# Kernel tuning notes

Measured on AMD Instinct MI355X. Metric: run time of the kernel, lower is better.

## Reference

```python
import math
import jax, jax.numpy as jnp
import numpy as np

B, S, E = 4, 2048, 768
H, D = 12, 64
LOCAL_H, GLOBAL_H = 8, 4
WINDOW_BASE, MIN_W, MAX_W = 128, 32, 512
GLOBAL_RATIO = 0.1
MASK_VALUE = -1e9


def setup_inputs() -> dict:
    key = jax.random.key(0)
    k1, k2, k3 = jax.random.split(key, 3)
    return {
        "x": jax.random.normal(k1, (B, S, E), dtype=jnp.float32),
        "w_attn": jax.random.normal(k2, (E, 3 * E), dtype=jnp.float32) * 0.02,
        "b_attn": jnp.zeros((3 * E,), dtype=jnp.float32),
        "w_proj": jax.random.normal(k3, (E, E), dtype=jnp.float32) * 0.02,
        "b_proj": jnp.zeros((E,), dtype=jnp.float32),
    }


def _masks(seq_len: int):
    # dynamic window (adaptive): base * sqrt(S/base), clamped
    w = int(WINDOW_BASE * math.sqrt(seq_len / WINDOW_BASE))
    w = max(MIN_W, min(w, MAX_W))
    half = w // 2
    i = jnp.arange(seq_len)[:, None]
    j = jnp.arange(seq_len)[None, :]
    # local: window band then causal override -> allowed iff i-half <= j <= i
    local_allowed = (j >= i - half) & (j <= i)
    local_mask = jnp.where(local_allowed, 0.0, MASK_VALUE).astype(jnp.float32)
    # global: columns at linspace positions allowed for all rows, plus full causal
    n_glob = max(1, int(seq_len * GLOBAL_RATIO))
    gpos = jnp.linspace(0.0, seq_len - 1, n_glob).astype(jnp.int32)
    is_gcol = jnp.zeros((seq_len,), dtype=bool).at[gpos].set(True)
    global_allowed = (j <= i) | is_gcol[None, :]
    global_mask = jnp.where(global_allowed, 0.0, MASK_VALUE).astype(jnp.float32)
    return local_mask, global_mask


def _attend(q, k, v, mask):
    # q,k,v: [B,h,S,D]; mask: [S,S]
    scale = 1.0 / math.sqrt(q.shape[-1])
    scores = jnp.einsum("bhqd,bhkd->bhqk", q, k) * scale + mask[None, None]
    w = jax.nn.softmax(scores, axis=-1)
    return jnp.einsum("bhqk,bhkd->bhqd", w, v)


def reference(x, w_attn, b_attn, w_proj, b_proj):
    b, s, _ = x.shape
    qkv = x @ w_attn + b_attn                       # [B,S,3E]
    q, k, v = jnp.split(qkv, 3, axis=-1)
    def heads(t):
        return t.reshape(b, s, H, D).transpose(0, 2, 1, 3)  # [B,H,S,D]
    q, k, v = heads(q), heads(k), heads(v)
    local_mask, global_mask = _masks(s)
    local_out = _attend(q[:, :LOCAL_H], k[:, :LOCAL_H], v[:, :LOCAL_H], local_mask)
    global_out = _attend(q[:, LOCAL_H:], k[:, LOCAL_H:], v[:, LOCAL_H:], global_mask)
    attn = jnp.concatenate([local_out, global_out], axis=1)  # heads 0..7 local, 8..11 global
    attn = attn.transpose(0, 2, 1, 3).reshape(b, s, E)
    return attn @ w_proj + b_proj
```

## Files before the change

### kernel.cpp

```cpp
#include <hip/hip_runtime.h>
#include <stdint.h>


#define NH 12
#define SQ 2048

typedef __bf16 bf16x8 __attribute__((ext_vector_type(8)));
typedef float f32x4 __attribute__((ext_vector_type(4)));

#define GLOAD_LDS16(g, l)                                                      \
  __builtin_amdgcn_global_load_lds(                                            \
      (__attribute__((address_space(1))) void*)(g),                            \
      (__attribute__((address_space(3))) void*)(l), 16, 0, 0)

__device__ __forceinline__ unsigned short bfbits(float f) {
  __bf16 h = (__bf16)f;
  return *(unsigned short*)&h;
}

__global__ __launch_bounds__(256) void prep(
    const float* __restrict__ x, unsigned short* __restrict__ xb,
    const float* __restrict__ w_attn, unsigned short* __restrict__ wattnT,
    const float* __restrict__ w_proj, unsigned short* __restrict__ wprojT) {
  const int bid = blockIdx.x, t = threadIdx.x;
  if (bid < 512) {
    const int n4 = 8192 * 768 / 4;
    for (int i = bid * 256 + t; i < n4; i += 512 * 256) {
      float4 v = ((const float4*)x)[i];
      ((ushort4*)xb)[i] = make_ushort4(bfbits(v.x), bfbits(v.y), bfbits(v.z), bfbits(v.w));
    }
    return;
  }
  __shared__ float tile[32][33];
  const float* in; unsigned short* out; int K, N, tl;
  if (bid < 512 + 72 * 24) { in = w_attn; out = wattnT; K = 768; N = 2304; tl = bid - 512; }
  else                     { in = w_proj; out = wprojT; K = 768; N = 768;  tl = bid - 512 - 72 * 24; }
  const int tpr = N / 32;
  const int n0 = (tl % tpr) * 32, k0 = (tl / tpr) * 32;
  const int tx = t & 31, ty = t >> 5;
  for (int r = ty; r < 32; r += 8) tile[r][tx] = in[(size_t)(k0 + r) * N + n0 + tx];
  __syncthreads();
  for (int r = ty; r < 32; r += 8) out[(size_t)(n0 + r) * K + k0 + tx] = bfbits(tile[tx][r]);
}

__global__ __launch_bounds__(256) void vprep(const unsigned short* __restrict__ QKV,
                                             unsigned short* __restrict__ Vtb,
                                             unsigned short* __restrict__ Kg,
                                             unsigned short* __restrict__ VgT,
                                             int* __restrict__ gidx) {
  const int id = blockIdx.x, t = threadIdx.x;
  if (id < 1536) {
    const int bh = id >> 5, b = bh / NH, h = bh % NH;
    const int s0 = (id & 31) * 64;
    __shared__ unsigned short T[64][72];
    const int r = t >> 2, c0 = (t & 3) * 16;
    const size_t src = (size_t)(b * SQ + s0 + r) * 2304 + 1536 + h * 64 + c0;
    *(uint4*)&T[r][c0]     = *(const uint4*)&QKV[src];
    *(uint4*)&T[r][c0 + 8] = *(const uint4*)&QKV[src + 8];
    __syncthreads();
    unsigned short pk[16];
#pragma unroll
    for (int z = 0; z < 16; ++z) pk[z] = T[c0 + z][r];
    size_t dst = (size_t)bh * 131072 + (size_t)r * 2048 + s0 + c0;
    *(uint4*)&Vtb[dst]     = *(uint4*)&pk[0];
    *(uint4*)&Vtb[dst + 8] = *(uint4*)&pk[8];
    return;
  }
  const int g = id - 1536;
  const int bh = g >> 3, y = g & 7;
  const int b = bh >> 2, h = 8 + (bh & 3);
  if (g == 0) {
    int c = t;
    gidx[c] = (c < 203) ? (int)((double)c * (2047.0 / 203.0)) : ((c == 203) ? 2047 : -1);
  }
  {
    int c = t, ch = y;
    int col = (c < 203) ? (int)((double)c * (2047.0 / 203.0)) : ((c == 203) ? 2047 : -1);
    uint4 v = {0u, 0u, 0u, 0u};
    if (col >= 0) v = *(const uint4*)&QKV[(size_t)(b * SQ + col) * 2304 + 768 + h * 64 + ch * 8];
    *(uint4*)&Kg[((size_t)bh * 256 + c) * 64 + ch * 8] = v;
  }
  {
    int d = t >> 2;
    int cb = (t & 3) * 64 + y * 8;
    for (int cc = 0; cc < 8; ++cc) {
      int c = cb + cc;
      int col = (c < 203) ? (int)((double)c * (2047.0 / 203.0)) : ((c == 203) ? 2047 : -1);
      unsigned short v = 0;
      if (col >= 0) v = QKV[(size_t)(b * SQ + col) * 2304 + 1536 + h * 64 + d];
      VgT[((size_t)bh * 64 + d) * 256 + c] = v;
    }
  }
}

__device__ __forceinline__ void gemm_mainloop(
    const unsigned short* __restrict__ A, const unsigned short* __restrict__ BT,
    int m0, int n0, int tid,
    unsigned short* As, unsigned short* Bs,
    f32x4 acc[4][4]) {
  const int lane = tid & 63, wave = tid >> 6;
  const int wm = wave >> 1, wn = wave & 1;
  const int ln = lane & 15, quad = lane >> 4;
  const int arow = wave * 16 + (lane >> 2);
  const int acol = (lane & 3) * 8;

#pragma unroll
  for (int mi = 0; mi < 4; ++mi)
#pragma unroll
    for (int ni = 0; ni < 4; ++ni) acc[mi][ni] = (f32x4){0.f, 0.f, 0.f, 0.f};

  for (int kt = 0; kt < 12; ++kt) {
    const int k0 = kt * 64;
    __syncthreads();
#pragma unroll
    for (int p = 0; p < 2; ++p) {
      const int ldso = (p * 64 + wave * 16) * 32;
      GLOAD_LDS16(A  + (size_t)(m0 + p * 64 + arow) * 768 + k0 + acol,       &As[ldso]);
      GLOAD_LDS16(A  + (size_t)(m0 + p * 64 + arow) * 768 + k0 + 32 + acol,  &As[4096 + ldso]);
      GLOAD_LDS16(BT + (size_t)(n0 + p * 64 + arow) * 768 + k0 + acol,       &Bs[ldso]);
      GLOAD_LDS16(BT + (size_t)(n0 + p * 64 + arow) * 768 + k0 + 32 + acol,  &Bs[4096 + ldso]);
    }
    __syncthreads();
#pragma unroll
    for (int kh = 0; kh < 2; ++kh) {
      const int base = kh * 4096;
      bf16x8 aF[4], bF[4];
#pragma unroll
      for (int mi = 0; mi < 4; ++mi)
        aF[mi] = *(const bf16x8*)&As[base + (wm * 64 + mi * 16 + ln) * 32 + quad * 8];
#pragma unroll
      for (int ni = 0; ni < 4; ++ni)
        bF[ni] = *(const bf16x8*)&Bs[base + (wn * 64 + ni * 16 + ln) * 32 + quad * 8];
#pragma unroll
      for (int mi = 0; mi < 4; ++mi)
#pragma unroll
        for (int ni = 0; ni < 4; ++ni)
          acc[mi][ni] = __builtin_amdgcn_mfma_f32_16x16x32_bf16(aF[mi], bF[ni], acc[mi][ni], 0, 0, 0);
    }
  }
}

__global__ __launch_bounds__(256) void qkv_gemm(
    const unsigned short* __restrict__ Xb, const unsigned short* __restrict__ WT,
    const float* __restrict__ bias, unsigned short* __restrict__ Out) {
  __shared__ __attribute__((aligned(16))) unsigned short As[2 * 128 * 32];
  __shared__ __attribute__((aligned(16))) unsigned short Bs[2 * 128 * 32];
  f32x4 acc[4][4];
  const int wg = (blockIdx.x & 7) * 144 + (blockIdx.x >> 3);
  const int m0 = (wg / 18) * 128, n0 = (wg % 18) * 128;
  const int tid = threadIdx.x;
  gemm_mainloop(Xb, WT, m0, n0, tid, As, Bs, acc);
  const int lane = tid & 63, wave = tid >> 6;
  const int wm = wave >> 1, wn = wave & 1, ln = lane & 15, quad = lane >> 4;
#pragma unroll
  for (int mi = 0; mi < 4; ++mi)
#pragma unroll
    for (int ni = 0; ni < 4; ++ni) {
      int n = n0 + wn * 64 + ni * 16 + ln;
      float bs = bias[n];
#pragma unroll
      for (int rg = 0; rg < 4; ++rg) {
        int m = m0 + wm * 64 + mi * 16 + quad * 4 + rg;
        Out[(size_t)m * 2304 + n] = bfbits(acc[mi][ni][rg] + bs);
      }
    }
}

__global__ __launch_bounds__(256) void proj_gemm(
    const unsigned short* __restrict__ Ab, const unsigned short* __restrict__ WT,
    const float* __restrict__ bias, float* __restrict__ Out) {
  __shared__ __attribute__((aligned(16))) unsigned short As[2 * 128 * 32];
  __shared__ __attribute__((aligned(16))) unsigned short Bs[2 * 128 * 32];
  f32x4 acc[4][4];
  const int wg = (blockIdx.x & 7) * 48 + (blockIdx.x >> 3);
  const int m0 = (wg / 6) * 128, n0 = (wg % 6) * 128;
  const int tid = threadIdx.x;
  gemm_mainloop(Ab, WT, m0, n0, tid, As, Bs, acc);
  const int lane = tid & 63, wave = tid >> 6;
  const int wm = wave >> 1, wn = wave & 1, ln = lane & 15, quad = lane >> 4;
#pragma unroll
  for (int mi = 0; mi < 4; ++mi)
#pragma unroll
    for (int ni = 0; ni < 4; ++ni)
#pragma unroll
      for (int rg = 0; rg < 4; ++rg) {
        int m = m0 + wm * 64 + mi * 16 + quad * 4 + rg;
        int n = n0 + wn * 64 + ni * 16 + ln;
        Out[(size_t)m * 768 + n] = acc[mi][ni][rg] + bias[n];
      }
}

__global__ __launch_bounds__(256, 4) void attn_kernel(
    const unsigned short* __restrict__ QKV,
    const unsigned short* __restrict__ Vtb,
    const unsigned short* __restrict__ Kg, const unsigned short* __restrict__ VgT,
    const int* __restrict__ gidx,
    unsigned short* __restrict__ AOut,
    unsigned short* __restrict__ Opart,
    float* __restrict__ Lpart) {
  __shared__ __attribute__((aligned(16))) unsigned short Ks[64 * 64];
  __shared__ __attribute__((aligned(16))) unsigned short Vs[64 * 64];
  __shared__ __attribute__((aligned(16))) unsigned short Ps[64 * 64];

  const int gid = blockIdx.x;
  int b, h, qb, vt0, vt1;
  bool multi = false;
  if (gid < 1536) {
    int bh = gid / 96, rem = gid % 96;
    b = bh >> 2; h = 8 + (bh & 3);
    int part;
    if (rem < 4)       { qb = rem;                               part = 0; }
    else if (rem < 20) { int z = rem - 4;  qb = 4 + (z >> 1);    part = z & 1; }
    else if (rem < 44) { int z = rem - 20; int q = z / 3; qb = 12 + q; part = z - 3 * q; }
    else if (rem < 76) { int z = rem - 44; qb = 20 + (z >> 2);   part = z & 3; }
    else               { int z = rem - 76; int q = z / 5; qb = 28 + q; part = z - 5 * q; }
    vt0 = part * 8;
    vt1 = min(vt0 + 8, qb + 5);
    multi = (qb >= 4);
  } else {
    int lid = gid - 1536;
    int bh = lid >> 5; b = bh >> 3; h = bh & 7; qb = lid & 31;
    vt0 = ((qb > 4) ? qb - 4 : 0) + 4;
    vt1 = qb + 5;
  }
  const int qb0 = qb * 64;
  const bool is_local = (h < 8);
  const int tid = threadIdx.x, lane = tid & 63, wave = tid >> 6;
  const int ln = lane & 15, quad = lane >> 4;
  const int bh48 = b * NH + h;
  const int bhg = (b << 2) | (h & 3);

  const size_t qoff = (size_t)(b * SQ + qb0 + wave * 16 + ln) * 2304 + h * 64;
  bf16x8 qA0 = *(const bf16x8*)&QKV[qoff + quad * 8];
  bf16x8 qA1 = *(const bf16x8*)&QKV[qoff + 32 + quad * 8];

  bf16x8 onesF;
#pragma unroll
  for (int z = 0; z < 8; ++z) onesF[z] = (__bf16)1.0f;

  f32x4 o[4];
  f32x4 ls = (f32x4){0.f, 0.f, 0.f, 0.f};
#pragma unroll
  for (int dt = 0; dt < 4; ++dt) o[dt] = (f32x4){0.f, 0.f, 0.f, 0.f};

  const int irow = qb0 + wave * 16 + quad * 4;
  const int iw = qb0 + wave * 16;
  const int sr = tid >> 3, sch = tid & 7;
  const int ssw = (sch ^ (sr & 7)) * 8;
  const int s0k = (quad ^ (ln & 7)) * 8;
  const int s1k = ((quad + 4) ^ (ln & 7)) * 8;
  const int lnh = ln >> 3, ln7 = ln & 7;

  const float S2 = 0.125f * 1.44269504f, B2 = 8.0f * 1.44269504f;

  uint4 pk0, pk1, pv0, pv1;
  auto issue_load = [&](int vt) {
    if (vt >= 4) {
      const int kstart = (vt - 4) * 64;
      const size_t ko = (size_t)(b * SQ + kstart + sr) * 2304 + 768 + h * 64 + sch * 8;
      pk0 = *(const uint4*)&QKV[ko];
      pk1 = *(const uint4*)&QKV[ko + (size_t)32 * 2304];
      const size_t vo = (size_t)bh48 * 131072 + (size_t)sr * 2048 + kstart + sch * 8;
      pv0 = *(const uint4*)&Vtb[vo];
      pv1 = *(const uint4*)&Vtb[vo + 32 * 2048];
    } else {
      const int kg0 = vt * 64;
      pk0 = *(const uint4*)&Kg[((size_t)bhg * 256 + kg0 + sr) * 64 + sch * 8];
      pk1 = *(const uint4*)&Kg[((size_t)bhg * 256 + kg0 + 32 + sr) * 64 + sch * 8];
      pv0 = *(const uint4*)&VgT[((size_t)bhg * 64 + sr) * 256 + kg0 + sch * 8];
      pv1 = *(const uint4*)&VgT[((size_t)bhg * 64 + 32 + sr) * 256 + kg0 + sch * 8];
    }
  };
  issue_load(vt0);

  for (int vt = vt0; vt < vt1; ++vt) {
    const bool gph = (vt < 4);
    __syncthreads();
    *(uint4*)&Ks[sr * 64 + ssw]        = pk0;
    *(uint4*)&Ks[(32 + sr) * 64 + ssw] = pk1;
    *(uint4*)&Vs[sr * 64 + ssw]        = pv0;
    *(uint4*)&Vs[(32 + sr) * 64 + ssw] = pv1;
    __syncthreads();
    if (vt + 1 < vt1) issue_load(vt + 1);

    const int kstart = (vt - 4) * 64;
    const int kg0 = vt * 64;
    float sc[4][4];
    const bool full = !gph && (kstart + 63 <= iw) && (!is_local || kstart >= iw - 241);
#pragma unroll
    for (int nt = 0; nt < 4; ++nt) {
      bf16x8 kF0 = *(const bf16x8*)&Ks[(nt * 16 + ln) * 64 + s0k];
      bf16x8 kF1 = *(const bf16x8*)&Ks[(nt * 16 + ln) * 64 + s1k];
      f32x4 c = (f32x4){0.f, 0.f, 0.f, 0.f};
      c = __builtin_amdgcn_mfma_f32_16x16x32_bf16(qA0, kF0, c, 0, 0, 0);
      c = __builtin_amdgcn_mfma_f32_16x16x32_bf16(qA1, kF1, c, 0, 0, 0);
      if (full) {
#pragma unroll
        for (int rg = 0; rg < 4; ++rg) sc[nt][rg] = c[rg] * S2 - B2;
      } else if (!gph) {
        int j = kstart + nt * 16 + ln;
#pragma unroll
        for (int rg = 0; rg < 4; ++rg) {
          int i = irow + rg;
          bool ok = is_local ? (j >= i - 256 && j <= i) : (j <= i);
          sc[nt][rg] = ok ? (c[rg] * S2 - B2) : -1e9f;
        }
      } else {
        int jg = gidx[kg0 + nt * 16 + ln];
#pragma unroll
        for (int rg = 0; rg < 4; ++rg) {
          bool ok = jg > (irow + rg);
          sc[nt][rg] = ok ? (c[rg] * S2 - B2) : -1e9f;
        }
      }
    }

    __bf16* P = (__bf16*)Ps;
#pragma unroll
    for (int rg = 0; rg < 4; ++rg) {
      int prow = wave * 16 + quad * 4 + rg;
      int pbase = prow * 64 + ln7;
      int pr7 = prow & 7;
#pragma unroll
      for (int nt = 0; nt < 4; ++nt)
        P[pbase + (((nt * 2 + lnh) ^ pr7) << 3)] = (__bf16)exp2f(sc[nt][rg]);
    }
    bf16x8 pF0 = *(const bf16x8*)&Ps[(wave * 16 + ln) * 64 + s0k];
    bf16x8 pF1 = *(const bf16x8*)&Ps[(wave * 16 + ln) * 64 + s1k];
    ls = __builtin_amdgcn_mfma_f32_16x16x32_bf16(pF0, onesF, ls, 0, 0, 0);
    ls = __builtin_amdgcn_mfma_f32_16x16x32_bf16(pF1, onesF, ls, 0, 0, 0);
#pragma unroll
    for (int dt = 0; dt < 4; ++dt) {
      bf16x8 vF0 = *(const bf16x8*)&Vs[(dt * 16 + ln) * 64 + s0k];
      bf16x8 vF1 = *(const bf16x8*)&Vs[(dt * 16 + ln) * 64 + s1k];
      o[dt] = __builtin_amdgcn_mfma_f32_16x16x32_bf16(pF0, vF0, o[dt], 0, 0, 0);
      o[dt] = __builtin_amdgcn_mfma_f32_16x16x32_bf16(pF1, vF1, o[dt], 0, 0, 0);
    }
  }

  if (gid >= 1536 || !multi) {
#pragma unroll
    for (int dt = 0; dt < 4; ++dt)
#pragma unroll
      for (int rg = 0; rg < 4; ++rg) {
        int row = b * SQ + qb0 + wave * 16 + quad * 4 + rg;
        int e = h * 64 + dt * 16 + ln;
        AOut[(size_t)row * 768 + e] = bfbits(o[dt][rg] / ls[rg]);
      }
  } else {
#pragma unroll
    for (int dt = 0; dt < 4; ++dt)
#pragma unroll
      for (int rg = 0; rg < 4; ++rg) {
        int row = wave * 16 + quad * 4 + rg;
        Opart[(size_t)gid * 4096 + row * 64 + dt * 16 + ln] = bfbits(o[dt][rg]);
      }
    if (ln == 0) {
#pragma unroll
      for (int rg = 0; rg < 4; ++rg)
        Lpart[(size_t)gid * 64 + wave * 16 + quad * 4 + rg] = ls[rg];
    }
  }
}

__global__ __launch_bounds__(256) void combine_parts(
    const unsigned short* __restrict__ Opart, const float* __restrict__ Lpart,
    unsigned short* __restrict__ AOut) {
  const int bid = blockIdx.x;
  const int bh = bid / 28, qb = bid % 28 + 4;
  const int b = bh >> 2, h = 8 + (bh & 3);
  int C, np;
  if (qb < 12)      { C = 2 * qb - 4;  np = 2; }
  else if (qb < 20) { C = 3 * qb - 16; np = 3; }
  else if (qb < 28) { C = 4 * qb - 36; np = 4; }
  else              { C = 5 * qb - 64; np = 5; }
  const int slot0 = bh * 96 + C;
  const int t = threadIdx.x, r = t >> 2, c0 = (t & 3) * 16;
  float acc[16];
#pragma unroll
  for (int z = 0; z < 16; ++z) acc[z] = 0.f;
  float l = 0.f;
  for (int p = 0; p < np; ++p) {
    const unsigned short* src = &Opart[(size_t)(slot0 + p) * 4096 + r * 64 + c0];
    bf16x8 v0 = *(const bf16x8*)&src[0];
    bf16x8 v1 = *(const bf16x8*)&src[8];
#pragma unroll
    for (int z = 0; z < 8; ++z) { acc[z] += (float)v0[z]; acc[8 + z] += (float)v1[z]; }
    l += Lpart[(size_t)(slot0 + p) * 64 + r];
  }
  float inv = 1.f / l;
  unsigned short pk[16];
#pragma unroll
  for (int z = 0; z < 16; ++z) pk[z] = bfbits(acc[z] * inv);
  size_t dst = (size_t)(b * SQ + qb * 64 + r) * 768 + h * 64 + c0;
  *(uint4*)&AOut[dst]     = *(uint4*)&pk[0];
  *(uint4*)&AOut[dst + 8] = *(uint4*)&pk[8];
}

extern "C" void kernel_launch(void* const* d_in, const int* in_sizes, int n_in,
                              void* d_out, int out_size, void* d_ws, size_t ws_size,
                              hipStream_t stream) {
  const float* x      = (const float*)d_in[0];
  const float* w_attn = (const float*)d_in[1];
  const float* b_attn = (const float*)d_in[2];
  const float* w_proj = (const float*)d_in[3];
  const float* b_proj = (const float*)d_in[4];
  float* out = (float*)d_out;

  char* ws = (char*)d_ws;
  size_t off = 0;
  auto alloc = [&](size_t bytes) {
    void* p = ws + off;
    off += (bytes + 255) & ~(size_t)255;
    return p;
  };
  unsigned short* xb     = (unsigned short*)alloc((size_t)8192 * 768 * 2);
  unsigned short* wattnT = (unsigned short*)alloc((size_t)2304 * 768 * 2);
  unsigned short* wprojT = (unsigned short*)alloc((size_t)768 * 768 * 2);
  unsigned short* qkvb   = (unsigned short*)alloc((size_t)8192 * 2304 * 2);
  unsigned short* Vtb    = (unsigned short*)alloc((size_t)48 * 64 * 2048 * 2);
  unsigned short* Kgb    = (unsigned short*)alloc((size_t)16 * 256 * 64 * 2);
  unsigned short* VgTb   = (unsigned short*)alloc((size_t)16 * 64 * 256 * 2);
  int* gidxb             = (int*)alloc((size_t)256 * 4);
  unsigned short* Opartb = (unsigned short*)alloc((size_t)1536 * 4096 * 2);
  float* Lpartb          = (float*)alloc((size_t)1536 * 64 * 4);
  unsigned short* attnb  = xb;

  prep<<<dim3(512 + 72 * 24 + 24 * 24), dim3(256), 0, stream>>>(
      x, xb, w_attn, wattnT, w_proj, wprojT);
  qkv_gemm<<<dim3(1152), dim3(256), 0, stream>>>(xb, wattnT, b_attn, qkvb);
  vprep<<<dim3(1536 + 128), dim3(256), 0, stream>>>(qkvb, Vtb, Kgb, VgTb, gidxb);
  attn_kernel<<<dim3(2560), dim3(256), 0, stream>>>(qkvb, Vtb, Kgb, VgTb, gidxb,
                                                    attnb, Opartb, Lpartb);
  combine_parts<<<dim3(448), dim3(256), 0, stream>>>(Opartb, Lpartb, attnb);
  proj_gemm<<<dim3(384), dim3(256), 0, stream>>>(attnb, wprojT, b_proj, out);
}
```

Baseline: 203.3 us.

## Replace QKV GEMM with 256x256-tile double-buffered swizzled-LDS kernel

Swaps the 128x128-tile QKV projection GEMM for a new kernel using 256x256 tiles, 512 threads and a 64-wide K slice. Loads are double-buffered, so the next K tile streams straight into LDS while MFMAs run on the current one. An XOR swizzle on the LDS layout is meant to avoid bank conflicts. The larger tile raises data reuse and cuts global traffic, but it uses 128 KB of LDS and 128 accumulator registers per lane, and launches only 288 workgroups, which is close to the CU count and may leave tail imbalance.

```diff
diff --git a/kernel.cpp b/kernel.cpp
--- a/kernel.cpp
+++ b/kernel.cpp
@@ -93,6 +93,78 @@
   }
 }
 
+__global__ __launch_bounds__(512, 2) void qkv_gemm256(
+    const unsigned short* __restrict__ Xb, const unsigned short* __restrict__ WT,
+    const float* __restrict__ bias, unsigned short* __restrict__ Out) {
+  __shared__ __attribute__((aligned(16))) unsigned short As[2][256 * 64];
+  __shared__ __attribute__((aligned(16))) unsigned short Bs[2][256 * 64];
+  const int tid = threadIdx.x, lane = tid & 63, wave = tid >> 6;
+  const int wg = (blockIdx.x & 7) * 36 + (blockIdx.x >> 3);
+  const int m0 = (wg / 9) * 256, n0 = (wg % 9) * 256;
+  const int ln = lane & 15, quad = lane >> 4;
+  const int wm = wave >> 2, wn = wave & 3;
+  const int srow = tid >> 3;
+  const int scol = ((tid & 7) ^ (srow & 7)) * 8;
+  const int ln7 = ln & 7;
+  const int sk0 = (quad ^ ln7) * 8;
+  const int sk1 = ((quad + 4) ^ ln7) * 8;
+
+  f32x4 acc[8][4];
+#pragma unroll
+  for (int mi = 0; mi < 8; ++mi)
+#pragma unroll
+    for (int ni = 0; ni < 4; ++ni) acc[mi][ni] = (f32x4){0.f, 0.f, 0.f, 0.f};
+
+  auto stage = [&](int kt, int buf) {
+    const int k0 = kt * 64;
+#pragma unroll
+    for (int i = 0; i < 4; ++i) {
+      GLOAD_LDS16(Xb + (size_t)(m0 + i * 64 + srow) * 768 + k0 + scol,
+                  &As[buf][(i * 512 + wave * 64) * 8]);
+      GLOAD_LDS16(WT + (size_t)(n0 + i * 64 + srow) * 768 + k0 + scol,
+                  &Bs[buf][(i * 512 + wave * 64) * 8]);
+    }
+  };
+
+  stage(0, 0);
+  __syncthreads();
+  int cur = 0;
+  for (int kt = 0; kt < 12; ++kt) {
+    if (kt + 1 < 12) stage(kt + 1, cur ^ 1);
+#pragma unroll
+    for (int kh = 0; kh < 2; ++kh) {
+      const int sk = kh ? sk1 : sk0;
+      bf16x8 aF[8], bF[4];
+#pragma unroll
+      for (int mi = 0; mi < 8; ++mi)
+        aF[mi] = *(const bf16x8*)&As[cur][(wm * 128 + mi * 16 + ln) * 64 + sk];
+#pragma unroll
+      for (int ni = 0; ni < 4; ++ni)
+        bF[ni] = *(const bf16x8*)&Bs[cur][(wn * 64 + ni * 16 + ln) * 64 + sk];
+#pragma unroll
+      for (int mi = 0; mi < 8; ++mi)
+#pragma unroll
+        for (int ni = 0; ni < 4; ++ni)
+          acc[mi][ni] = __builtin_amdgcn_mfma_f32_16x16x32_bf16(aF[mi], bF[ni], acc[mi][ni], 0, 0, 0);
+    }
+    __syncthreads();
+    cur ^= 1;
+  }
+
+#pragma unroll
+  for (int mi = 0; mi < 8; ++mi)
+#pragma unroll
+    for (int ni = 0; ni < 4; ++ni) {
+      int n = n0 + wn * 64 + ni * 16 + ln;
+      float bs = bias[n];
+#pragma unroll
+      for (int rg = 0; rg < 4; ++rg) {
+        int m = m0 + wm * 128 + mi * 16 + quad * 4 + rg;
+        Out[(size_t)m * 2304 + n] = bfbits(acc[mi][ni][rg] + bs);
+      }
+    }
+}
+
 __device__ __forceinline__ void gemm_mainloop(
     const unsigned short* __restrict__ A, const unsigned short* __restrict__ BT,
     int m0, int n0, int tid,
@@ -138,32 +210,6 @@
           acc[mi][ni] = __builtin_amdgcn_mfma_f32_16x16x32_bf16(aF[mi], bF[ni], acc[mi][ni], 0, 0, 0);
     }
   }
-}
-
-__global__ __launch_bounds__(256) void qkv_gemm(
-    const unsigned short* __restrict__ Xb, const unsigned short* __restrict__ WT,
-    const float* __restrict__ bias, unsigned short* __restrict__ Out) {
-  __shared__ __attribute__((aligned(16))) unsigned short As[2 * 128 * 32];
-  __shared__ __attribute__((aligned(16))) unsigned short Bs[2 * 128 * 32];
-  f32x4 acc[4][4];
-  const int wg = (blockIdx.x & 7) * 144 + (blockIdx.x >> 3);
-  const int m0 = (wg / 18) * 128, n0 = (wg % 18) * 128;
-  const int tid = threadIdx.x;
-  gemm_mainloop(Xb, WT, m0, n0, tid, As, Bs, acc);
-  const int lane = tid & 63, wave = tid >> 6;
-  const int wm = wave >> 1, wn = wave & 1, ln = lane & 15, quad = lane >> 4;
-#pragma unroll
-  for (int mi = 0; mi < 4; ++mi)
-#pragma unroll
-    for (int ni = 0; ni < 4; ++ni) {
-      int n = n0 + wn * 64 + ni * 16 + ln;
-      float bs = bias[n];
-#pragma unroll
-      for (int rg = 0; rg < 4; ++rg) {
-        int m = m0 + wm * 64 + mi * 16 + quad * 4 + rg;
-        Out[(size_t)m * 2304 + n] = bfbits(acc[mi][ni][rg] + bs);
-      }
-    }
 }
 
 __global__ __launch_bounds__(256) void proj_gemm(
@@ -428,7 +474,7 @@
 
   prep<<<dim3(512 + 72 * 24 + 24 * 24), dim3(256), 0, stream>>>(
       x, xb, w_attn, wattnT, w_proj, wprojT);
-  qkv_gemm<<<dim3(1152), dim3(256), 0, stream>>>(xb, wattnT, b_attn, qkvb);
+  qkv_gemm256<<<dim3(288), dim3(512), 0, stream>>>(xb, wattnT, b_attn, qkvb);
   vprep<<<dim3(1536 + 128), dim3(256), 0, stream>>>(qkvb, Vtb, Kgb, VgTb, gidxb);
   attn_kernel<<<dim3(2560), dim3(256), 0, stream>>>(qkvb, Vtb, Kgb, VgTb, gidxb,
                                                     attnb, Opartb, Lpartb);
```

New measurement: 218.6 us. 1.08x slower.

## Double-buffer GEMM mainloop with XOR-swizzled LDS layout and prefetch

Applied to the files above, without the earlier changes.

Rewrites the shared GEMM mainloop used by the QKV and output projections so the next K tile is prefetched into a second LDS buffer while the current one feeds the MFMAs. The tile is stored as 64-wide rows with an XOR swizzle to avoid LDS bank conflicts, and raw barriers, waitcnt and setprio control the overlap. LDS use per block doubles, and launch bounds now request two blocks per CU. The last iteration issues a redundant reload of tile 11, and the hand-placed waitcnt counts must match the number of loads in flight.

```diff
diff --git a/kernel.cpp b/kernel.cpp
--- a/kernel.cpp
+++ b/kernel.cpp
@@ -100,51 +100,66 @@
     f32x4 acc[4][4]) {
   const int lane = tid & 63, wave = tid >> 6;
   const int wm = wave >> 1, wn = wave & 1;
-  const int ln = lane & 15, quad = lane >> 4;
-  const int arow = wave * 16 + (lane >> 2);
-  const int acol = (lane & 3) * 8;
+  const int ln = lane & 15, quad = lane >> 4, ln7 = lane & 7;
+  const int srow = tid >> 3;
+  const int scol = ((tid & 7) ^ (srow & 7)) * 8;
+  const int sbase = wave * 512;
 
 #pragma unroll
   for (int mi = 0; mi < 4; ++mi)
 #pragma unroll
     for (int ni = 0; ni < 4; ++ni) acc[mi][ni] = (f32x4){0.f, 0.f, 0.f, 0.f};
 
+  auto stage = [&](int kt, int buf) {
+    const int k0 = kt * 64;
+    const int bo = buf * 8192;
+#pragma unroll
+    for (int rr = 0; rr < 4; ++rr) {
+      GLOAD_LDS16(A  + (size_t)(m0 + rr * 32 + srow) * 768 + k0 + scol,
+                  &As[bo + rr * 2048 + sbase]);
+      GLOAD_LDS16(BT + (size_t)(n0 + rr * 32 + srow) * 768 + k0 + scol,
+                  &Bs[bo + rr * 2048 + sbase]);
+    }
+  };
+
+  stage(0, 0);
+  int buf = 0;
   for (int kt = 0; kt < 12; ++kt) {
-    const int k0 = kt * 64;
-    __syncthreads();
-#pragma unroll
-    for (int p = 0; p < 2; ++p) {
-      const int ldso = (p * 64 + wave * 16) * 32;
-      GLOAD_LDS16(A  + (size_t)(m0 + p * 64 + arow) * 768 + k0 + acol,       &As[ldso]);
-      GLOAD_LDS16(A  + (size_t)(m0 + p * 64 + arow) * 768 + k0 + 32 + acol,  &As[4096 + ldso]);
-      GLOAD_LDS16(BT + (size_t)(n0 + p * 64 + arow) * 768 + k0 + acol,       &Bs[ldso]);
-      GLOAD_LDS16(BT + (size_t)(n0 + p * 64 + arow) * 768 + k0 + 32 + acol,  &Bs[4096 + ldso]);
-    }
-    __syncthreads();
+    stage(kt < 11 ? kt + 1 : 11, buf ^ 1);
+    asm volatile("s_waitcnt vmcnt(8)" ::: "memory");
+    __builtin_amdgcn_sched_barrier(0);
+    __builtin_amdgcn_s_barrier();
+    __builtin_amdgcn_s_setprio(1);
+    const int bo = buf * 8192;
 #pragma unroll
     for (int kh = 0; kh < 2; ++kh) {
-      const int base = kh * 4096;
+      const int sk = ((kh * 4 + quad) ^ ln7) * 8;
       bf16x8 aF[4], bF[4];
 #pragma unroll
       for (int mi = 0; mi < 4; ++mi)
-        aF[mi] = *(const bf16x8*)&As[base + (wm * 64 + mi * 16 + ln) * 32 + quad * 8];
+        aF[mi] = *(const bf16x8*)&As[bo + (wm * 64 + mi * 16 + ln) * 64 + sk];
 #pragma unroll
       for (int ni = 0; ni < 4; ++ni)
-        bF[ni] = *(const bf16x8*)&Bs[base + (wn * 64 + ni * 16 + ln) * 32 + quad * 8];
+        bF[ni] = *(const bf16x8*)&Bs[bo + (wn * 64 + ni * 16 + ln) * 64 + sk];
 #pragma unroll
       for (int mi = 0; mi < 4; ++mi)
 #pragma unroll
         for (int ni = 0; ni < 4; ++ni)
           acc[mi][ni] = __builtin_amdgcn_mfma_f32_16x16x32_bf16(aF[mi], bF[ni], acc[mi][ni], 0, 0, 0);
     }
-  }
-}
-
-__global__ __launch_bounds__(256) void qkv_gemm(
+    __builtin_amdgcn_s_setprio(0);
+    asm volatile("s_waitcnt lgkmcnt(0)" ::: "memory");
+    __builtin_amdgcn_sched_barrier(0);
+    __builtin_amdgcn_s_barrier();
+    buf ^= 1;
+  }
+}
+
+__global__ __launch_bounds__(256, 2) void qkv_gemm(
     const unsigned short* __restrict__ Xb, const unsigned short* __restrict__ WT,
     const float* __restrict__ bias, unsigned short* __restrict__ Out) {
-  __shared__ __attribute__((aligned(16))) unsigned short As[2 * 128 * 32];
-  __shared__ __attribute__((aligned(16))) unsigned short Bs[2 * 128 * 32];
+  __shared__ __attribute__((aligned(16))) unsigned short As[2 * 128 * 64];
+  __shared__ __attribute__((aligned(16))) unsigned short Bs[2 * 128 * 64];
   f32x4 acc[4][4];
   const int wg = (blockIdx.x & 7) * 144 + (blockIdx.x >> 3);
   const int m0 = (wg / 18) * 128, n0 = (wg % 18) * 128;
@@ -166,11 +181,11 @@
     }
 }
 
-__global__ __launch_bounds__(256) void proj_gemm(
+__global__ __launch_bounds__(256, 2) void proj_gemm(
     const unsigned short* __restrict__ Ab, const unsigned short* __restrict__ WT,
     const float* __restrict__ bias, float* __restrict__ Out) {
-  __shared__ __attribute__((aligned(16))) unsigned short As[2 * 128 * 32];
-  __shared__ __attribute__((aligned(16))) unsigned short Bs[2 * 128 * 32];
+  __shared__ __attribute__((aligned(16))) unsigned short As[2 * 128 * 64];
+  __shared__ __attribute__((aligned(16))) unsigned short Bs[2 * 128 * 64];
   f32x4 acc[4][4];
   const int wg = (blockIdx.x & 7) * 48 + (blockIdx.x >> 3);
   const int m0 = (wg / 6) * 128, n0 = (wg % 6) * 128;
```

Result: slower. 209.0 us (+2.8%).
